# Kernel tuning notes

Hardware: AMD Instinct MI355X
Metric: run time of the kernel (lower is better)

## Reference

```python
import jax, jax.numpy as jnp
import numpy as np

HID = 512
EMB = 768
TOP_K = 8
LN_EPS = 1e-5
NORM_EPS = 1e-12


def _mlp_ln(x, W1, b1, W2, b2, g, beta):
    # Linear -> ReLU -> Linear -> LayerNorm
    h = jax.nn.relu(x @ W1 + b1)
    h = h @ W2 + b2
    mu = jnp.mean(h, axis=-1, keepdims=True)
    var = jnp.var(h, axis=-1, keepdims=True)
    return (h - mu) * jax.lax.rsqrt(var + LN_EPS) * g + beta


def _l2norm(x):
    n = jnp.linalg.norm(x, axis=-1, keepdims=True)
    return x / jnp.maximum(n, NORM_EPS)


def setup_inputs() -> dict:
    key = jax.random.key(0)
    ks = jax.random.split(key, 12)
    s_in = 1.0 / np.sqrt(EMB)
    s_h = 1.0 / np.sqrt(HID)
    inp = {
        "query_embeddings": jax.random.normal(ks[0], (64, 32, EMB), jnp.float32),
        "doc_embeddings": jax.random.normal(ks[1], (50000, 16, EMB), jnp.float32),
        "qW1": jax.random.normal(ks[2], (EMB, HID), jnp.float32) * s_in,
        "qb1": jnp.zeros((HID,), jnp.float32),
        "qW2": jax.random.normal(ks[3], (HID, HID), jnp.float32) * s_h,
        "qb2": jnp.zeros((HID,), jnp.float32),
        "qg": jnp.ones((HID,), jnp.float32),
        "qbeta": jnp.zeros((HID,), jnp.float32),
        "dW1": jax.random.normal(ks[4], (EMB, HID), jnp.float32) * s_in,
        "db1": jnp.zeros((HID,), jnp.float32),
        "dW2": jax.random.normal(ks[5], (HID, HID), jnp.float32) * s_h,
        "db2": jnp.zeros((HID,), jnp.float32),
        "dg": jnp.ones((HID,), jnp.float32),
        "dbeta": jnp.zeros((HID,), jnp.float32),
        "pW": jax.random.normal(ks[6], (HID, HID), jnp.float32) * s_h,
        "pb": jnp.zeros((HID,), jnp.float32),
        "temperature": jnp.asarray(1.0, jnp.float32),
    }
    return inp


def reference(query_embeddings, doc_embeddings, qW1, qb1, qW2, qb2, qg, qbeta,
              dW1, db1, dW2, db2, dg, dbeta, pW, pb, temperature):
    # Mean-pool over token dims, encode with MLP+LayerNorm
    q_repr = _mlp_ln(query_embeddings.mean(axis=1), qW1, qb1, qW2, qb2, qg, qbeta)  # [B,H]
    d_repr = _mlp_ln(doc_embeddings.mean(axis=1), dW1, db1, dW2, db2, dg, dbeta)    # [N,H]
    q_norm = _l2norm(q_repr @ pW + pb)
    d_norm = _l2norm(d_repr @ pW + pb)
    scores = (q_norm @ d_norm.T) / temperature  # [B,N]
    top_k_scores, top_k_indices = jax.lax.top_k(scores, TOP_K)  # [B,K]
    retrieved_docs = doc_embeddings[top_k_indices]  # [B,K,doc_len,EMB]
    return top_k_scores, retrieved_docs
```

## Files before the change

### kernel.cpp

```cpp
#include <hip/hip_runtime.h>

#define NQ 64
#define ND 50000
#define NDP 50048
#define MT (NDP + NQ)
#define QTOK 32
#define DTOK 16
#define EMB 768
#define HID 512

typedef short s16x8 __attribute__((ext_vector_type(8)));
typedef float f32x4 __attribute__((ext_vector_type(4)));

__device__ __forceinline__ unsigned short f2bf(float f) {
    union { float f; unsigned u; } x; x.f = f;
    unsigned r = x.u + 0x7fffu + ((x.u >> 16) & 1u);
    return (unsigned short)(r >> 16);
}
__device__ __forceinline__ float bf2f(unsigned short h) {
    union { unsigned u; float f; } x; x.u = ((unsigned)h) << 16;
    return x.f;
}
__device__ __forceinline__ unsigned packhi2(float a, float b) {
    return (unsigned)f2bf(a) | ((unsigned)f2bf(b) << 16);
}
__device__ __forceinline__ unsigned packlo2(float a, float b) {
    unsigned short ha = f2bf(a), hb = f2bf(b);
    return (unsigned)f2bf(a - bf2f(ha)) | ((unsigned)f2bf(b - bf2f(hb)) << 16);
}

__device__ __forceinline__ void gload_lds16(const void* g, void* l) {
    __builtin_amdgcn_global_load_lds(
        (const __attribute__((address_space(1))) void*)g,
        (__attribute__((address_space(3))) void*)l, 16, 0, 0);
}


__global__ void pool_aug_all(const float* __restrict__ de, const float* __restrict__ qe,
                             ushort* __restrict__ out) {
    int blk = blockIdx.x, t = threadIdx.x;
    const float* src;
    int T;
    size_t orow;
    if (blk < ND) { src = de + (size_t)blk * DTOK * EMB; T = DTOK; orow = blk; }
    else          { int qr = blk - ND; src = qe + (size_t)qr * QTOK * EMB; T = QTOK; orow = NDP + qr; }
    const float4* ip = (const float4*)src + t;
    float4 a = make_float4(0.f, 0.f, 0.f, 0.f);
    for (int i = 0; i < T; ++i) {
        float4 v = ip[(size_t)i * (EMB / 4)];
        a.x += v.x; a.y += v.y; a.z += v.z; a.w += v.w;
    }
    const float s = 1.0f / (float)T;
    float v0 = a.x * s, v1 = a.y * s, v2 = a.z * s, v3 = a.w * s;
    ushort* base = out + orow * (2 * EMB);
    *(uint2*)(base + t * 4)       = make_uint2(packhi2(v0, v1), packhi2(v2, v3));
    *(uint2*)(base + EMB + t * 4) = make_uint2(packlo2(v0, v1), packlo2(v2, v3));
}

__global__ void wconv(const float* __restrict__ W, ushort* __restrict__ Wp, int K) {
    int n = blockIdx.x;
    ushort* base = Wp + (size_t)n * 2 * K;
    for (int k = threadIdx.x; k < K; k += blockDim.x) {
        float v = W[(size_t)k * HID + n];
        unsigned short hi = f2bf(v);
        base[k]     = hi;
        base[K + k] = f2bf(v - bf2f(hi));
    }
}

template <int MODE>
__global__ __launch_bounds__(512, 4) void mfma_gemm2(const ushort* __restrict__ A,
                                                     const ushort* __restrict__ Bd,
                                                     const ushort* __restrict__ Bq,
                                                     const float* __restrict__ biasd,
                                                     const float* __restrict__ biasq,
                                                     void* __restrict__ out,
                                                     int M, int K) {
    __shared__ ushort As[128 * 64];
    __shared__ ushort Bs[256 * 64];
    const int Ks = 2 * K;
    const int bm = blockIdx.x * 128;
    const int bn = blockIdx.y * 256;
    const bool isq = (bm >= NDP);
    const ushort* B = isq ? Bq : Bd;
    const float* bias = isq ? biasq : biasd;
    const int tid = threadIdx.x;
    const int lane = tid & 63;
    const int wave = tid >> 6;
    const int wr = wave >> 2;
    const int wc = wave & 3;
    f32x4 acc[4][4] = {};

    for (int k0 = 0; k0 < 3 * K; k0 += 64) {
        const int ka = (k0 < 2 * K) ? k0 : k0 - 2 * K;
        const int kb = (k0 < K) ? k0 : k0 - K;
        #pragma unroll
        for (int c = 0; c < 2; ++c) {
            int idx = c * 512 + tid;
            int row = idx >> 3, s = idx & 7;
            int gr = bm + row; if (gr >= M) gr = M - 1;
            int ks = (s ^ (row & 7)) << 3;
            gload_lds16(A + (size_t)gr * Ks + ka + ks, As + idx * 8);
        }
        #pragma unroll
        for (int c = 0; c < 4; ++c) {
            int idx = c * 512 + tid;
            int n = idx >> 3, s = idx & 7;
            int ks = (s ^ (n & 7)) << 3;
            gload_lds16(B + (size_t)(bn + n) * Ks + kb + ks, Bs + idx * 8);
        }
        __syncthreads();

        #pragma unroll
        for (int kk = 0; kk < 2; ++kk) {
            const int sp = kk * 4 + (lane >> 4);
            s16x8 a[4], b[4];
            #pragma unroll
            for (int i = 0; i < 4; ++i) {
                int r = wr * 64 + i * 16 + (lane & 15);
                a[i] = *(const s16x8*)(As + r * 64 + ((sp ^ (r & 7)) << 3));
            }
            #pragma unroll
            for (int j = 0; j < 4; ++j) {
                int n = wc * 64 + j * 16 + (lane & 15);
                b[j] = *(const s16x8*)(Bs + n * 64 + ((sp ^ (n & 7)) << 3));
            }
            #pragma unroll
            for (int i = 0; i < 4; ++i)
                #pragma unroll
                for (int j = 0; j < 4; ++j)
                    acc[i][j] = __builtin_amdgcn_mfma_f32_16x16x32_bf16(a[i], b[j], acc[i][j], 0, 0, 0);
        }
        __syncthreads();
    }

    #pragma unroll
    for (int j = 0; j < 4; ++j) {
        int col = bn + wc * 64 + j * 16 + (lane & 15);
        float bv = bias[col];
        #pragma unroll
        for (int i = 0; i < 4; ++i) {
            #pragma unroll
            for (int r = 0; r < 4; ++r) {
                int grow = bm + wr * 64 + i * 16 + ((lane >> 4) << 2) + r;
                if (grow >= M) continue;
                float v = acc[i][j][r] + bv;
                if (MODE == 1) {
                    v = fmaxf(v, 0.0f);
                    unsigned short hi = f2bf(v);
                    ushort* op = (ushort*)out + (size_t)grow * (2 * HID);
                    op[col]       = hi;
                    op[HID + col] = f2bf(v - bf2f(hi));
                } else {
                    ((float*)out)[(size_t)grow * HID + col] = v;
                }
            }
        }
    }
}

__global__ __launch_bounds__(512, 4) void mfma_scores(const ushort* __restrict__ A,
                                                      const ushort* __restrict__ B,
                                                      float* __restrict__ out,
                                                      int M, int N_B, int K, long ldo,
                                                      const float* __restrict__ temp) {
    __shared__ ushort As[128 * 64];
    __shared__ ushort Bs[256 * 64];
    const int Ks = 2 * K;
    const int bm = blockIdx.x * 128;
    const int bn = blockIdx.y * 256;
    const int tid = threadIdx.x;
    const int lane = tid & 63;
    const int wave = tid >> 6;
    const int wr = wave >> 2;
    const int wc = wave & 3;
    f32x4 acc[4][4] = {};

    for (int k0 = 0; k0 < 3 * K; k0 += 64) {
        const int ka = (k0 < 2 * K) ? k0 : k0 - 2 * K;
        const int kb = (k0 < K) ? k0 : k0 - K;
        #pragma unroll
        for (int c = 0; c < 2; ++c) {
            int idx = c * 512 + tid;
            int row = idx >> 3, s = idx & 7;
            int gr = bm + row; if (gr >= M) gr = M - 1;
            int ks = (s ^ (row & 7)) << 3;
            gload_lds16(A + (size_t)gr * Ks + ka + ks, As + idx * 8);
        }
        #pragma unroll
        for (int c = 0; c < 4; ++c) {
            int idx = c * 512 + tid;
            int n = idx >> 3, s = idx & 7;
            int gn = bn + n; if (gn >= N_B) gn = N_B - 1;
            int ks = (s ^ (n & 7)) << 3;
            gload_lds16(B + (size_t)gn * Ks + kb + ks, Bs + idx * 8);
        }
        __syncthreads();

        #pragma unroll
        for (int kk = 0; kk < 2; ++kk) {
            const int sp = kk * 4 + (lane >> 4);
            s16x8 a[4], b[4];
            #pragma unroll
            for (int i = 0; i < 4; ++i) {
                int r = wr * 64 + i * 16 + (lane & 15);
                a[i] = *(const s16x8*)(As + r * 64 + ((sp ^ (r & 7)) << 3));
            }
            #pragma unroll
            for (int j = 0; j < 4; ++j) {
                int n = wc * 64 + j * 16 + (lane & 15);
                b[j] = *(const s16x8*)(Bs + n * 64 + ((sp ^ (n & 7)) << 3));
            }
            #pragma unroll
            for (int i = 0; i < 4; ++i)
                #pragma unroll
                for (int j = 0; j < 4; ++j)
                    acc[i][j] = __builtin_amdgcn_mfma_f32_16x16x32_bf16(a[i], b[j], acc[i][j], 0, 0, 0);
        }
        __syncthreads();
    }

    float invT = 1.0f / temp[0];
    #pragma unroll
    for (int j = 0; j < 4; ++j) {
        int gcol = bn + wc * 64 + j * 16 + (lane & 15);
        #pragma unroll
        for (int i = 0; i < 4; ++i)
            #pragma unroll
            for (int r = 0; r < 4; ++r) {
                int grow = bm + wr * 64 + i * 16 + ((lane >> 4) << 2) + r;
                if (grow < M && gcol < N_B)
                    out[(size_t)grow * ldo + gcol] = acc[i][j][r] * invT;
            }
    }
}

__device__ __forceinline__ void store_hilo(ushort* __restrict__ base, int lane,
                                           float v0, float v1, float v2, float v3,
                                           float v4, float v5, float v6, float v7) {
    *(uint4*)(base + lane * 8) =
        make_uint4(packhi2(v0, v1), packhi2(v2, v3), packhi2(v4, v5), packhi2(v6, v7));
    *(uint4*)(base + HID + lane * 8) =
        make_uint4(packlo2(v0, v1), packlo2(v2, v3), packlo2(v4, v5), packlo2(v6, v7));
}

__global__ __launch_bounds__(256) void ln_aug(const float* __restrict__ x,
                                              const float* __restrict__ dg,
                                              const float* __restrict__ dbe,
                                              const float* __restrict__ qg,
                                              const float* __restrict__ qbe,
                                              ushort* __restrict__ out, int M) {
    int wv = threadIdx.x >> 6, lane = threadIdx.x & 63;
    int row = blockIdx.x * 4 + wv;
    if (row >= M) return;
    const float* g  = (row >= NDP) ? qg  : dg;
    const float* be = (row >= NDP) ? qbe : dbe;
    const float4* p = (const float4*)(x + (size_t)row * HID);
    float4 a = p[lane * 2], b = p[lane * 2 + 1];
    float s  = a.x + a.y + a.z + a.w + b.x + b.y + b.z + b.w;
    float sq = a.x*a.x + a.y*a.y + a.z*a.z + a.w*a.w
             + b.x*b.x + b.y*b.y + b.z*b.z + b.w*b.w;
    #pragma unroll
    for (int o = 32; o > 0; o >>= 1) { s += __shfl_xor(s, o); sq += __shfl_xor(sq, o); }
    float mu  = s * (1.0f / HID);
    float var = sq * (1.0f / HID) - mu * mu;
    float r   = rsqrtf(var + 1e-5f);
    const float4* gp = (const float4*)g;
    const float4* bp = (const float4*)be;
    float4 g0 = gp[lane * 2], g1 = gp[lane * 2 + 1];
    float4 b0 = bp[lane * 2], b1 = bp[lane * 2 + 1];
    store_hilo(out + (size_t)row * (2 * HID), lane,
               (a.x - mu) * r * g0.x + b0.x, (a.y - mu) * r * g0.y + b0.y,
               (a.z - mu) * r * g0.z + b0.z, (a.w - mu) * r * g0.w + b0.w,
               (b.x - mu) * r * g1.x + b1.x, (b.y - mu) * r * g1.y + b1.y,
               (b.z - mu) * r * g1.z + b1.z, (b.w - mu) * r * g1.w + b1.w);
}

__global__ __launch_bounds__(256) void l2_aug(const float* __restrict__ x,
                                              ushort* __restrict__ out, int M) {
    int wv = threadIdx.x >> 6, lane = threadIdx.x & 63;
    int row = blockIdx.x * 4 + wv;
    if (row >= M) return;
    const float4* p = (const float4*)(x + (size_t)row * HID);
    float4 a = p[lane * 2], b = p[lane * 2 + 1];
    float sq = a.x*a.x + a.y*a.y + a.z*a.z + a.w*a.w
             + b.x*b.x + b.y*b.y + b.z*b.z + b.w*b.w;
    #pragma unroll
    for (int o = 32; o > 0; o >>= 1) sq += __shfl_xor(sq, o);
    float n = sqrtf(sq);
    float r = 1.0f / fmaxf(n, 1e-12f);
    store_hilo(out + (size_t)row * (2 * HID), lane,
               a.x * r, a.y * r, a.z * r, a.w * r,
               b.x * r, b.y * r, b.z * r, b.w * r);
}

__global__ __launch_bounds__(256) void topk_kernel(const float* __restrict__ scores,
                                                   float* __restrict__ out_scores,
                                                   int* __restrict__ out_idx, int N) {
    __shared__ float ls[2048];
    __shared__ int   li[2048];
    const int q   = blockIdx.x;
    const int tid = threadIdx.x;
    const float* row = scores + (size_t)q * N;
    float s[8]; int ix[8];
    #pragma unroll
    for (int i = 0; i < 8; ++i) { s[i] = -1e30f; ix[i] = 0x7fffffff; }
    for (int j = tid; j < N; j += 256) {
        float v = row[j];
        if (v > s[7]) {
            s[7] = v; ix[7] = j;
            #pragma unroll
            for (int t = 7; t > 0; --t) {
                bool sw = (s[t] > s[t-1]) || (s[t] == s[t-1] && ix[t] < ix[t-1]);
                if (sw) {
                    float tv = s[t]; s[t] = s[t-1]; s[t-1] = tv;
                    int   ti = ix[t]; ix[t] = ix[t-1]; ix[t-1] = ti;
                }
            }
        }
    }
    #pragma unroll
    for (int i = 0; i < 8; ++i) { ls[tid * 8 + i] = s[i]; li[tid * 8 + i] = ix[i]; }
    __syncthreads();
    for (int w = 64; w >= 1; w >>= 2) {
        if (tid < w) {
            #pragma unroll
            for (int i = 0; i < 8; ++i) { s[i] = -1e30f; ix[i] = 0x7fffffff; }
            #pragma unroll
            for (int c = 0; c < 32; ++c) {
                float v  = ls[tid * 32 + c];
                int   vi = li[tid * 32 + c];
                bool better = (v > s[7]) || (v == s[7] && vi < ix[7]);
                if (better) {
                    s[7] = v; ix[7] = vi;
                    #pragma unroll
                    for (int t = 7; t > 0; --t) {
                        bool sw = (s[t] > s[t-1]) || (s[t] == s[t-1] && ix[t] < ix[t-1]);
                        if (sw) {
                            float tv = s[t]; s[t] = s[t-1]; s[t-1] = tv;
                            int   ti = ix[t]; ix[t] = ix[t-1]; ix[t-1] = ti;
                        }
                    }
                }
            }
        }
        __syncthreads();
        if (tid < w) {
            #pragma unroll
            for (int i = 0; i < 8; ++i) { ls[tid * 8 + i] = s[i]; li[tid * 8 + i] = ix[i]; }
        }
        __syncthreads();
    }
    if (tid < 8) {
        out_scores[(size_t)q * 8 + tid] = ls[tid];
        out_idx[q * 8 + tid]            = li[tid];
    }
}

__global__ __launch_bounds__(256) void gather_kernel(const float* __restrict__ docs,
                                                     const int* __restrict__ idx,
                                                     float* __restrict__ out) {
    const int b = blockIdx.x;
    const int d = idx[b];
    const float4* src = (const float4*)(docs + (size_t)d * DTOK * EMB);
    float4*       dst = (float4*)(out + (size_t)b * DTOK * EMB);
    for (int i = threadIdx.x; i < DTOK * EMB / 4; i += 256) dst[i] = src[i];
}

extern "C" void kernel_launch(void* const* d_in, const int* in_sizes, int n_in,
                              void* d_out, int out_size, void* d_ws, size_t ws_size,
                              hipStream_t stream) {
    const float* qe   = (const float*)d_in[0];
    const float* de   = (const float*)d_in[1];
    const float* qW1  = (const float*)d_in[2];
    const float* qb1  = (const float*)d_in[3];
    const float* qW2  = (const float*)d_in[4];
    const float* qb2  = (const float*)d_in[5];
    const float* qg   = (const float*)d_in[6];
    const float* qbe  = (const float*)d_in[7];
    const float* dW1  = (const float*)d_in[8];
    const float* db1  = (const float*)d_in[9];
    const float* dW2  = (const float*)d_in[10];
    const float* db2  = (const float*)d_in[11];
    const float* dg   = (const float*)d_in[12];
    const float* dbe  = (const float*)d_in[13];
    const float* pW   = (const float*)d_in[14];
    const float* pb   = (const float*)d_in[15];
    const float* temp = (const float*)d_in[16];

    float* out = (float*)d_out;

    char* w = (char*)d_ws;
    float*  scores = (float*)w;                 w += (size_t)NQ * ND * 4;
    ushort* W1p    = (ushort*)w;                w += (size_t)HID * 2 * EMB * 2;
    ushort* W2p    = (ushort*)w;                w += (size_t)HID * 2 * HID * 2;
    ushort* pWp    = (ushort*)w;                w += (size_t)HID * 2 * HID * 2;
    ushort* QW1p   = (ushort*)w;                w += (size_t)HID * 2 * EMB * 2;
    ushort* QW2p   = (ushort*)w;                w += (size_t)HID * 2 * HID * 2;
    int*    tidx   = (int*)w;                   w += 4096;
    ushort* pooled = (ushort*)w;                w += (size_t)MT * 2 * EMB * 2;
    ushort* h1a    = (ushort*)w;                w += (size_t)MT * 2 * HID * 2;
    float*  h2     = (float*)w;                 w += (size_t)MT * HID * 4;
    ushort* lna    = pooled;
    float*  pproj  = h2;
    ushort* Daug   = h1a;
    ushort* qaug   = Daug + (size_t)NDP * 2 * HID;

    const int GM = (MT + 127) / 128;

    wconv<<<HID, 256, 0, stream>>>(dW1, W1p, EMB);
    wconv<<<HID, 256, 0, stream>>>(dW2, W2p, HID);
    wconv<<<HID, 256, 0, stream>>>(pW,  pWp, HID);
    wconv<<<HID, 256, 0, stream>>>(qW1, QW1p, EMB);
    wconv<<<HID, 256, 0, stream>>>(qW2, QW2p, HID);

    pool_aug_all<<<ND + NQ, 192, 0, stream>>>(de, qe, pooled);
    mfma_gemm2<1><<<dim3(GM, 2), 512, 0, stream>>>(pooled, W1p, QW1p, db1, qb1, h1a, MT, EMB);
    mfma_gemm2<0><<<dim3(GM, 2), 512, 0, stream>>>(h1a, W2p, QW2p, db2, qb2, h2, MT, HID);
    ln_aug<<<(MT + 3) / 4, 256, 0, stream>>>(h2, dg, dbe, qg, qbe, lna, MT);
    mfma_gemm2<0><<<dim3(GM, 2), 512, 0, stream>>>(lna, pWp, pWp, pb, pb, pproj, MT, HID);
    l2_aug<<<(MT + 3) / 4, 256, 0, stream>>>(pproj, Daug, MT);

    mfma_scores<<<dim3(1, (ND + 255) / 256), 512, 0, stream>>>(qaug, Daug, scores,
                                                               NQ, ND, HID, (long)ND, temp);

    topk_kernel<<<NQ, 256, 0, stream>>>(scores, out, tidx, ND);
    gather_kernel<<<NQ * 8, 256, 0, stream>>>(de, tidx, out + NQ * 8);
}
```

Before: 1.353 ms.

## Fold LayerNorm and L2 normalization into GEMM epilogues via precomputed row stats

Removes the separate ln_aug and l2_aug kernels. The second GEMM now emits raw hi/lo bf16 activations plus per-row partial sums and sums of squares. The projection GEMM uses gamma-prescaled weights and precomputed u/v vectors to apply LayerNorm algebraically in its epilogue, and writes partial L2 norms. The scores kernel then divides by those norms. This avoids fp32 round trips of the MT x 512 intermediates through memory and two extra launches. The cost is extra epilogue reductions and the numerics of computing variance from E[x^2]-mu^2 on unnormalized values, which can lose precision.

```diff
diff --git a/kernel.cpp b/kernel.cpp
--- a/kernel.cpp
+++ b/kernel.cpp
@@ -57,14 +57,58 @@
     *(uint2*)(base + EMB + t * 4) = make_uint2(packlo2(v0, v1), packlo2(v2, v3));
 }
 
-__global__ void wconv(const float* __restrict__ W, ushort* __restrict__ Wp, int K) {
-    int n = blockIdx.x;
-    ushort* base = Wp + (size_t)n * 2 * K;
+__global__ void wconv_all(const float* __restrict__ dW1, const float* __restrict__ qW1,
+                          const float* __restrict__ dW2, const float* __restrict__ qW2,
+                          const float* __restrict__ pW,
+                          const float* __restrict__ dg, const float* __restrict__ qg,
+                          ushort* __restrict__ W1p, ushort* __restrict__ QW1p,
+                          ushort* __restrict__ W2p, ushort* __restrict__ QW2p,
+                          ushort* __restrict__ W3d, ushort* __restrict__ W3q) {
+    int n = blockIdx.x, seg = blockIdx.y;
+    const float* W; const float* scale = nullptr; ushort* o; int K;
+    switch (seg) {
+        case 0:  W = dW1; o = W1p;  K = EMB; break;
+        case 1:  W = qW1; o = QW1p; K = EMB; break;
+        case 2:  W = dW2; o = W2p;  K = HID; break;
+        case 3:  W = qW2; o = QW2p; K = HID; break;
+        case 4:  W = pW;  o = W3d;  K = HID; scale = dg; break;
+        default: W = pW;  o = W3q;  K = HID; scale = qg; break;
+    }
+    ushort* base = o + (size_t)n * 2 * K;
     for (int k = threadIdx.x; k < K; k += blockDim.x) {
         float v = W[(size_t)k * HID + n];
+        if (scale) v *= scale[k];
         unsigned short hi = f2bf(v);
         base[k]     = hi;
         base[K + k] = f2bf(v - bf2f(hi));
+    }
+}
+
+__global__ void uv_prep(const float* __restrict__ pW, const float* __restrict__ pb,
+                        const float* __restrict__ dg, const float* __restrict__ dbe,
+                        const float* __restrict__ qg, const float* __restrict__ qbe,
+                        float* __restrict__ ud, float* __restrict__ vvd,
+                        float* __restrict__ uq, float* __restrict__ vvq) {
+    int n = blockIdx.x;
+    float a = 0.f, b = 0.f, c = 0.f, d = 0.f;
+    for (int k = threadIdx.x; k < HID; k += 256) {
+        float w = pW[(size_t)k * HID + n];
+        a += dg[k] * w; b += dbe[k] * w; c += qg[k] * w; d += qbe[k] * w;
+    }
+    #pragma unroll
+    for (int o = 32; o > 0; o >>= 1) {
+        a += __shfl_xor(a, o); b += __shfl_xor(b, o);
+        c += __shfl_xor(c, o); d += __shfl_xor(d, o);
+    }
+    __shared__ float red[4][4];
+    int wv = threadIdx.x >> 6, ln = threadIdx.x & 63;
+    if (ln == 0) { red[wv][0] = a; red[wv][1] = b; red[wv][2] = c; red[wv][3] = d; }
+    __syncthreads();
+    if (threadIdx.x == 0) {
+        float A = 0, B = 0, C = 0, D = 0;
+        #pragma unroll
+        for (int i = 0; i < 4; ++i) { A += red[i][0]; B += red[i][1]; C += red[i][2]; D += red[i][3]; }
+        ud[n] = A; vvd[n] = B + pb[n]; uq[n] = C; vvq[n] = D + pb[n];
     }
 }
 
@@ -72,18 +116,24 @@
 __global__ __launch_bounds__(512, 4) void mfma_gemm2(const ushort* __restrict__ A,
                                                      const ushort* __restrict__ Bd,
                                                      const ushort* __restrict__ Bq,
-                                                     const float* __restrict__ biasd,
-                                                     const float* __restrict__ biasq,
+                                                     const float* __restrict__ pard,
+                                                     const float* __restrict__ parq,
+                                                     const float* __restrict__ auxd,
+                                                     const float* __restrict__ auxq,
+                                                     const float2* __restrict__ statsIn,
+                                                     float2* __restrict__ sumsOut,
+                                                     float* __restrict__ normpOut,
                                                      void* __restrict__ out,
                                                      int M, int K) {
     __shared__ ushort As[128 * 64];
     __shared__ ushort Bs[256 * 64];
+    __shared__ float redS[4][128];
+    __shared__ float redQ[4][128];
     const int Ks = 2 * K;
     const int bm = blockIdx.x * 128;
     const int bn = blockIdx.y * 256;
     const bool isq = (bm >= NDP);
     const ushort* B = isq ? Bq : Bd;
-    const float* bias = isq ? biasq : biasd;
     const int tid = threadIdx.x;
     const int lane = tid & 63;
     const int wave = tid >> 6;
@@ -134,36 +184,112 @@
         __syncthreads();
     }
 
-    #pragma unroll
-    for (int j = 0; j < 4; ++j) {
-        int col = bn + wc * 64 + j * 16 + (lane & 15);
-        float bv = bias[col];
-        #pragma unroll
-        for (int i = 0; i < 4; ++i) {
-            #pragma unroll
-            for (int r = 0; r < 4; ++r) {
-                int grow = bm + wr * 64 + i * 16 + ((lane >> 4) << 2) + r;
-                if (grow >= M) continue;
-                float v = acc[i][j][r] + bv;
-                if (MODE == 1) {
-                    v = fmaxf(v, 0.0f);
+    if (MODE == 1 || MODE == 2) {
+        const float* bias = isq ? parq : pard;
+        float bv[4];
+        #pragma unroll
+        for (int j = 0; j < 4; ++j) bv[j] = bias[bn + wc * 64 + j * 16 + (lane & 15)];
+
+        if (MODE == 2) {
+            #pragma unroll
+            for (int i = 0; i < 4; ++i)
+                #pragma unroll
+                for (int r = 0; r < 4; ++r) {
+                    float ps = 0.f, pq = 0.f;
+                    #pragma unroll
+                    for (int j = 0; j < 4; ++j) {
+                        float v = acc[i][j][r] + bv[j];
+                        ps += v; pq += v * v;
+                    }
+                    #pragma unroll
+                    for (int o = 1; o < 16; o <<= 1) { ps += __shfl_xor(ps, o); pq += __shfl_xor(pq, o); }
+                    if ((lane & 15) == 0) {
+                        int rl = wr * 64 + i * 16 + ((lane >> 4) << 2) + r;
+                        redS[wc][rl] = ps; redQ[wc][rl] = pq;
+                    }
+                }
+            __syncthreads();
+            if (tid < 128) {
+                float s = redS[0][tid] + redS[1][tid] + redS[2][tid] + redS[3][tid];
+                float q = redQ[0][tid] + redQ[1][tid] + redQ[2][tid] + redQ[3][tid];
+                int grow = bm + tid;
+                if (grow < M) sumsOut[(size_t)grow * 2 + blockIdx.y] = make_float2(s, q);
+            }
+        }
+
+        #pragma unroll
+        for (int j = 0; j < 4; ++j) {
+            int col = bn + wc * 64 + j * 16 + (lane & 15);
+            #pragma unroll
+            for (int i = 0; i < 4; ++i)
+                #pragma unroll
+                for (int r = 0; r < 4; ++r) {
+                    int grow = bm + wr * 64 + i * 16 + ((lane >> 4) << 2) + r;
+                    if (grow >= M) continue;
+                    float v = acc[i][j][r] + bv[j];
+                    if (MODE == 1) v = fmaxf(v, 0.0f);
                     unsigned short hi = f2bf(v);
                     ushort* op = (ushort*)out + (size_t)grow * (2 * HID);
                     op[col]       = hi;
                     op[HID + col] = f2bf(v - bf2f(hi));
-                } else {
-                    ((float*)out)[(size_t)grow * HID + col] = v;
                 }
-            }
+        }
+    } else {
+        const float* u  = isq ? parq : pard;
+        const float* vv = isq ? auxq : auxd;
+        float uj[4], vj[4];
+        #pragma unroll
+        for (int j = 0; j < 4; ++j) {
+            int col = bn + wc * 64 + j * 16 + (lane & 15);
+            uj[j] = u[col]; vj[j] = vv[col];
+        }
+        #pragma unroll
+        for (int i = 0; i < 4; ++i)
+            #pragma unroll
+            for (int r = 0; r < 4; ++r) {
+                int grow = bm + wr * 64 + i * 16 + ((lane >> 4) << 2) + r;
+                int gsr  = grow < M ? grow : M - 1;
+                float2 p0 = statsIn[(size_t)gsr * 2 + 0];
+                float2 p1 = statsIn[(size_t)gsr * 2 + 1];
+                float s  = p0.x + p1.x, qq = p0.y + p1.y;
+                float mu  = s * (1.0f / 512.0f);
+                float var = qq * (1.0f / 512.0f) - mu * mu;
+                float rs  = rsqrtf(var + 1e-5f);
+                float ps = 0.f;
+                #pragma unroll
+                for (int j = 0; j < 4; ++j) {
+                    float val = rs * (acc[i][j][r] - mu * uj[j]) + vj[j];
+                    ps += val * val;
+                    if (grow < M) {
+                        int col = bn + wc * 64 + j * 16 + (lane & 15);
+                        unsigned short hi = f2bf(val);
+                        ushort* op = (ushort*)out + (size_t)grow * (2 * HID);
+                        op[col]       = hi;
+                        op[HID + col] = f2bf(val - bf2f(hi));
+                    }
+                }
+                #pragma unroll
+                for (int o = 1; o < 16; o <<= 1) ps += __shfl_xor(ps, o);
+                if ((lane & 15) == 0) {
+                    int rl = wr * 64 + i * 16 + ((lane >> 4) << 2) + r;
+                    redS[wc][rl] = ps;
+                }
+            }
+        __syncthreads();
+        if (tid < 128) {
+            float s = redS[0][tid] + redS[1][tid] + redS[2][tid] + redS[3][tid];
+            int grow = bm + tid;
+            if (grow < M) normpOut[(size_t)grow * 2 + blockIdx.y] = s;
         }
     }
 }
 
 __global__ __launch_bounds__(512, 4) void mfma_scores(const ushort* __restrict__ A,
                                                       const ushort* __restrict__ B,
+                                                      const float* __restrict__ normp,
                                                       float* __restrict__ out,
                                                       int M, int N_B, int K, long ldo,
-                                                      const float* __restrict__ temp) {
+                                                      const float* __restrict__ temp, int rowOff) {
     __shared__ ushort As[128 * 64];
     __shared__ ushort Bs[256 * 64];
     const int Ks = 2 * K;
@@ -221,77 +347,29 @@
     }
 
     float invT = 1.0f / temp[0];
+    float rB[4];
     #pragma unroll
     for (int j = 0; j < 4; ++j) {
         int gcol = bn + wc * 64 + j * 16 + (lane & 15);
-        #pragma unroll
-        for (int i = 0; i < 4; ++i)
-            #pragma unroll
-            for (int r = 0; r < 4; ++r) {
-                int grow = bm + wr * 64 + i * 16 + ((lane >> 4) << 2) + r;
+        int gc = gcol < N_B ? gcol : N_B - 1;
+        float n2 = normp[(size_t)gc * 2] + normp[(size_t)gc * 2 + 1];
+        rB[j] = 1.0f / fmaxf(sqrtf(n2), 1e-12f);
+    }
+    #pragma unroll
+    for (int i = 0; i < 4; ++i)
+        #pragma unroll
+        for (int r = 0; r < 4; ++r) {
+            int grow = bm + wr * 64 + i * 16 + ((lane >> 4) << 2) + r;
+            int gr = grow < M ? grow : M - 1;
+            float n2a = normp[(size_t)(rowOff + gr) * 2] + normp[(size_t)(rowOff + gr) * 2 + 1];
+            float rA = 1.0f / fmaxf(sqrtf(n2a), 1e-12f);
+            #pragma unroll
+            for (int j = 0; j < 4; ++j) {
+                int gcol = bn + wc * 64 + j * 16 + (lane & 15);
                 if (grow < M && gcol < N_B)
-                    out[(size_t)grow * ldo + gcol] = acc[i][j][r] * invT;
-            }
-    }
-}
-
-__device__ __forceinline__ void store_hilo(ushort* __restrict__ base, int lane,
-                                           float v0, float v1, float v2, float v3,
-                                           float v4, float v5, float v6, float v7) {
-    *(uint4*)(base + lane * 8) =
-        make_uint4(packhi2(v0, v1), packhi2(v2, v3), packhi2(v4, v5), packhi2(v6, v7));
-    *(uint4*)(base + HID + lane * 8) =
-        make_uint4(packlo2(v0, v1), packlo2(v2, v3), packlo2(v4, v5), packlo2(v6, v7));
-}
-
-__global__ __launch_bounds__(256) void ln_aug(const float* __restrict__ x,
-                                              const float* __restrict__ dg,
-                                              const float* __restrict__ dbe,
-                                              const float* __restrict__ qg,
-                                              const float* __restrict__ qbe,
-                                              ushort* __restrict__ out, int M) {
-    int wv = threadIdx.x >> 6, lane = threadIdx.x & 63;
-    int row = blockIdx.x * 4 + wv;
-    if (row >= M) return;
-    const float* g  = (row >= NDP) ? qg  : dg;
-    const float* be = (row >= NDP) ? qbe : dbe;
-    const float4* p = (const float4*)(x + (size_t)row * HID);
-    float4 a = p[lane * 2], b = p[lane * 2 + 1];
-    float s  = a.x + a.y + a.z + a.w + b.x + b.y + b.z + b.w;
-    float sq = a.x*a.x + a.y*a.y + a.z*a.z + a.w*a.w
-             + b.x*b.x + b.y*b.y + b.z*b.z + b.w*b.w;
-    #pragma unroll
-    for (int o = 32; o > 0; o >>= 1) { s += __shfl_xor(s, o); sq += __shfl_xor(sq, o); }
-    float mu  = s * (1.0f / HID);
-    float var = sq * (1.0f / HID) - mu * mu;
-    float r   = rsqrtf(var + 1e-5f);
-    const float4* gp = (const float4*)g;
-    const float4* bp = (const float4*)be;
-    float4 g0 = gp[lane * 2], g1 = gp[lane * 2 + 1];
-    float4 b0 = bp[lane * 2], b1 = bp[lane * 2 + 1];
-    store_hilo(out + (size_t)row * (2 * HID), lane,
-               (a.x - mu) * r * g0.x + b0.x, (a.y - mu) * r * g0.y + b0.y,
-               (a.z - mu) * r * g0.z + b0.z, (a.w - mu) * r * g0.w + b0.w,
-               (b.x - mu) * r * g1.x + b1.x, (b.y - mu) * r * g1.y + b1.y,
-               (b.z - mu) * r * g1.z + b1.z, (b.w - mu) * r * g1.w + b1.w);
-}
-
-__global__ __launch_bounds__(256) void l2_aug(const float* __restrict__ x,
-                                              ushort* __restrict__ out, int M) {
-    int wv = threadIdx.x >> 6, lane = threadIdx.x & 63;
-    int row = blockIdx.x * 4 + wv;
-    if (row >= M) return;
-    const float4* p = (const float4*)(x + (size_t)row * HID);
-    float4 a = p[lane * 2], b = p[lane * 2 + 1];
-    float sq = a.x*a.x + a.y*a.y + a.z*a.z + a.w*a.w
-             + b.x*b.x + b.y*b.y + b.z*b.z + b.w*b.w;
-    #pragma unroll
-    for (int o = 32; o > 0; o >>= 1) sq += __shfl_xor(sq, o);
-    float n = sqrtf(sq);
-    float r = 1.0f / fmaxf(n, 1e-12f);
-    store_hilo(out + (size_t)row * (2 * HID), lane,
-               a.x * r, a.y * r, a.z * r, a.w * r,
-               b.x * r, b.y * r, b.z * r, b.w * r);
+                    out[(size_t)grow * ldo + gcol] = acc[i][j][r] * rA * rB[j] * invT;
+            }
+        }
 }
 
 __global__ __launch_bounds__(256) void topk_kernel(const float* __restrict__ scores,
@@ -394,35 +472,42 @@
     float*  scores = (float*)w;                 w += (size_t)NQ * ND * 4;
     ushort* W1p    = (ushort*)w;                w += (size_t)HID * 2 * EMB * 2;
     ushort* W2p    = (ushort*)w;                w += (size_t)HID * 2 * HID * 2;
-    ushort* pWp    = (ushort*)w;                w += (size_t)HID * 2 * HID * 2;
+    ushort* W3d    = (ushort*)w;                w += (size_t)HID * 2 * HID * 2;
     ushort* QW1p   = (ushort*)w;                w += (size_t)HID * 2 * EMB * 2;
     ushort* QW2p   = (ushort*)w;                w += (size_t)HID * 2 * HID * 2;
+    ushort* W3q    = (ushort*)w;                w += (size_t)HID * 2 * HID * 2;
+    float*  ud     = (float*)w;                 w += HID * 4;
+    float*  vvd    = (float*)w;                 w += HID * 4;
+    float*  uq     = (float*)w;                 w += HID * 4;
+    float*  vvq    = (float*)w;                 w += HID * 4;
+    float2* sums   = (float2*)w;                w += (size_t)MT * 2 * 8;
+    float*  normp  = (float*)w;                 w += (size_t)MT * 2 * 4;
     int*    tidx   = (int*)w;                   w += 4096;
     ushort* pooled = (ushort*)w;                w += (size_t)MT * 2 * EMB * 2;
     ushort* h1a    = (ushort*)w;                w += (size_t)MT * 2 * HID * 2;
-    float*  h2     = (float*)w;                 w += (size_t)MT * HID * 4;
-    ushort* lna    = pooled;
-    float*  pproj  = h2;
+    ushort* h2a    = pooled;
     ushort* Daug   = h1a;
     ushort* qaug   = Daug + (size_t)NDP * 2 * HID;
 
     const int GM = (MT + 127) / 128;
 
-    wconv<<<HID, 256, 0, stream>>>(dW1, W1p, EMB);
-    wconv<<<HID, 256, 0, stream>>>(dW2, W2p, HID);
-    wconv<<<HID, 256, 0, stream>>>(pW,  pWp, HID);
-    wconv<<<HID, 256, 0, stream>>>(qW1, QW1p, EMB);
-    wconv<<<HID, 256, 0, stream>>>(qW2, QW2p, HID);
+    wconv_all<<<dim3(512, 6), 256, 0, stream>>>(dW1, qW1, dW2, qW2, pW, dg, qg,
+                                                W1p, QW1p, W2p, QW2p, W3d, W3q);
+    uv_prep<<<512, 256, 0, stream>>>(pW, pb, dg, dbe, qg, qbe, ud, vvd, uq, vvq);
 
     pool_aug_all<<<ND + NQ, 192, 0, stream>>>(de, qe, pooled);
-    mfma_gemm2<1><<<dim3(GM, 2), 512, 0, stream>>>(pooled, W1p, QW1p, db1, qb1, h1a, MT, EMB);
-    mfma_gemm2<0><<<dim3(GM, 2), 512, 0, stream>>>(h1a, W2p, QW2p, db2, qb2, h2, MT, HID);
-    ln_aug<<<(MT + 3) / 4, 256, 0, stream>>>(h2, dg, dbe, qg, qbe, lna, MT);
-    mfma_gemm2<0><<<dim3(GM, 2), 512, 0, stream>>>(lna, pWp, pWp, pb, pb, pproj, MT, HID);
-    l2_aug<<<(MT + 3) / 4, 256, 0, stream>>>(pproj, Daug, MT);
-
-    mfma_scores<<<dim3(1, (ND + 255) / 256), 512, 0, stream>>>(qaug, Daug, scores,
-                                                               NQ, ND, HID, (long)ND, temp);
+    mfma_gemm2<1><<<dim3(GM, 2), 512, 0, stream>>>(pooled, W1p, QW1p, db1, qb1,
+                                                   nullptr, nullptr, nullptr, nullptr, nullptr,
+                                                   h1a, MT, EMB);
+    mfma_gemm2<2><<<dim3(GM, 2), 512, 0, stream>>>(h1a, W2p, QW2p, db2, qb2,
+                                                   nullptr, nullptr, nullptr, sums, nullptr,
+                                                   h2a, MT, HID);
+    mfma_gemm2<3><<<dim3(GM, 2), 512, 0, stream>>>(h2a, W3d, W3q, ud, uq,
+                                                   vvd, vvq, sums, nullptr, normp,
+                                                   Daug, MT, HID);
+
+    mfma_scores<<<dim3(1, (ND + 255) / 256), 512, 0, stream>>>(qaug, Daug, normp, scores,
+                                                               NQ, ND, HID, (long)ND, temp, NDP);
 
     topk_kernel<<<NQ, 256, 0, stream>>>(scores, out, tidx, ND);
     gather_kernel<<<NQ * 8, 256, 0, stream>>>(de, tidx, out + NQ * 8);
```

After: 1.299 ms, median of 2. 4.0% less time.
